# Optimization experiments

Hardware: AMD Instinct MI355X
Metric: run time of the kernel (lower is better)

## Reference

```python
import jax, jax.numpy as jnp
import numpy as np

TEMP = 0.07


def setup_inputs() -> dict:
    key = jax.random.key(0)
    k1, k2 = jax.random.split(key)
    N, C = 8192, 512
    X = jax.random.normal(k1, (N, C), dtype=jnp.float32)
    Y = jax.random.normal(k2, (N, C), dtype=jnp.float32)
    return {"X": X, "Y": Y}


def reference(X, Y):
    # Original loop computes, per row i, cross-entropy over logits
    # [X_i.Y_i, X_i.Y_j (j != i)] / temp with label 0 (the positive).
    # Softmax CE is permutation-invariant, so this equals
    #   logsumexp(S_i / temp) - S_ii / temp,  S = X @ Y^T,
    # summed over rows (loop accumulates with +=, i.e. sum reduction).
    S = jnp.einsum('nc,mc->nm', X, Y) / TEMP  # [N, N]
    lse = jax.nn.logsumexp(S, axis=1)          # [N]
    pos = jnp.diagonal(S)                      # [N]
    return jnp.sum(lse - pos)
```

## Files before the change

### kernel.cpp

```cpp
#include <hip/hip_runtime.h>
#include <stdint.h>

#define N 8192
#define C 512
#define BM 128
#define BN 128
#define NSPLIT 8
#define COLS_PER_SPLIT (N / NSPLIT)
#define CT (COLS_PER_SPLIT / BN)
#define GRID_GEMM (64 * NSPLIT)
#define KSTEPS (C / 64)
#define U_SCALE 20.609929155556617f
#define LN2 0.6931471805599453f

typedef __attribute__((ext_vector_type(4)))  int   i32x4;
typedef __attribute__((ext_vector_type(8)))  int   i32x8;
typedef __attribute__((ext_vector_type(16))) float f32x16;

__global__ __launch_bounds__(256) void prep_kernel(const float* __restrict__ X,
                                                   const float* __restrict__ Y,
                                                   unsigned char* __restrict__ Xf8,
                                                   unsigned char* __restrict__ Yf8,
                                                   float* __restrict__ pos) {
  const int wave = threadIdx.x >> 6;
  const int lane = threadIdx.x & 63;
  const int row = blockIdx.x * 4 + wave;
  const float4* xr = (const float4*)(X + (size_t)row * C) + lane * 2;
  const float4* yr = (const float4*)(Y + (size_t)row * C) + lane * 2;
  float4 x0 = xr[0], x1 = xr[1];
  float4 y0 = yr[0], y1 = yr[1];
  float s = x0.x * y0.x + x0.y * y0.y + x0.z * y0.z + x0.w * y0.w
          + x1.x * y1.x + x1.y * y1.y + x1.z * y1.z + x1.w * y1.w;
  int2 ox, oy;
  ox.x = __builtin_amdgcn_cvt_pk_fp8_f32(x0.x, x0.y, 0, false);
  ox.x = __builtin_amdgcn_cvt_pk_fp8_f32(x0.z, x0.w, ox.x, true);
  ox.y = __builtin_amdgcn_cvt_pk_fp8_f32(x1.x, x1.y, 0, false);
  ox.y = __builtin_amdgcn_cvt_pk_fp8_f32(x1.z, x1.w, ox.y, true);
  oy.x = __builtin_amdgcn_cvt_pk_fp8_f32(y0.x, y0.y, 0, false);
  oy.x = __builtin_amdgcn_cvt_pk_fp8_f32(y0.z, y0.w, oy.x, true);
  oy.y = __builtin_amdgcn_cvt_pk_fp8_f32(y1.x, y1.y, 0, false);
  oy.y = __builtin_amdgcn_cvt_pk_fp8_f32(y1.z, y1.w, oy.y, true);
  ((int2*)(Xf8 + (size_t)row * C))[lane] = ox;
  ((int2*)(Yf8 + (size_t)row * C))[lane] = oy;
#pragma unroll
  for (int off = 32; off >= 1; off >>= 1) s += __shfl_xor(s, off);
  if (lane == 0) pos[row] = s * U_SCALE;
}

__global__ __launch_bounds__(256, 2) void gemm_lse_kernel(const unsigned char* __restrict__ Xf8,
                                                          const unsigned char* __restrict__ Yf8,
                                                          float2* __restrict__ partials) {
  __shared__ unsigned char Bs[4096 * 16];

  const int tid = threadIdx.x;
  const int bx = blockIdx.x;
  const int split = bx & (NSPLIT - 1);
  const int rb = bx >> 3;
  const int row0 = rb * BM;
  const int colbase = split * COLS_PER_SPLIT;

  const int w = tid >> 6;
  const int lane = tid & 63;
  const int lrow = lane & 31;
  const int h = lane >> 5;
  const int arow = w * 32 + lrow;

  i32x8 a_frag[KSTEPS];
#pragma unroll
  for (int s = 0; s < KSTEPS; ++s) {
    const unsigned char* ga = Xf8 + (size_t)(row0 + arow) * C + s * 64 + h * 32;
    i32x4 lo = *(const i32x4*)ga;
    i32x4 hi = *(const i32x4*)(ga + 16);
    a_frag[s] = i32x8{ lo[0], lo[1], lo[2], lo[3], hi[0], hi[1], hi[2], hi[3] };
  }

  float m_s[16], l_s[16];
#pragma unroll
  for (int s = 0; s < 16; ++s) { m_s[s] = -INFINITY; l_s[s] = 0.0f; }

  const unsigned char* bsr = &Bs[0] + lane * 16;

  for (int ct = 0; ct < CT; ++ct) {
    const int col0 = colbase + ct * BN;
    f32x16 acc[4];
#pragma unroll
    for (int t = 0; t < 4; ++t)
#pragma unroll
      for (int e = 0; e < 16; ++e) acc[t][e] = 0.0f;

#pragma unroll
    for (int t = 0; t < 16; ++t) {
      const int L  = t * 256 + tid;
      const int l6 = L & 63;
      const int q  = (L >> 6) & 1;
      const int tj = (L >> 7) & 3;
      const int s  = L >> 9;
      const unsigned char* gb = Yf8
          + (size_t)(col0 + tj * 32 + (l6 & 31)) * C
          + s * 64 + (l6 >> 5) * 32 + q * 16;
      uint32_t loff = (uint32_t)((t * 256 + (tid & ~63)) * 16);
      __builtin_amdgcn_global_load_lds(
          (const __attribute__((address_space(1))) uint32_t*)(uintptr_t)gb,
          (__attribute__((address_space(3))) uint32_t*)(uintptr_t)((char*)&Bs[0] + loff),
          16, 0, 0);
    }
    __syncthreads();

#pragma unroll
    for (int s = 0; s < KSTEPS; ++s) {
#pragma unroll
      for (int tj = 0; tj < 4; ++tj) {
        i32x4 blo = *(const i32x4*)(bsr + (s * 4 + tj) * 2048);
        i32x4 bhi = *(const i32x4*)(bsr + (s * 4 + tj) * 2048 + 1024);
        i32x8 bf = { blo[0], blo[1], blo[2], blo[3], bhi[0], bhi[1], bhi[2], bhi[3] };
        acc[tj] = __builtin_amdgcn_mfma_scale_f32_32x32x64_f8f6f4(
            a_frag[s], bf, acc[tj], 0, 0, 0, 127, 0, 127);
      }
    }

#pragma unroll
    for (int r = 0; r < 16; ++r) {
      float v0 = acc[0][r] * U_SCALE;
      float v1 = acc[1][r] * U_SCALE;
      float v2 = acc[2][r] * U_SCALE;
      float v3 = acc[3][r] * U_SCALE;
      float mx = fmaxf(fmaxf(v0, v1), fmaxf(v2, v3));
      float mn = fmaxf(m_s[r], mx);
      l_s[r] = l_s[r] * exp2f(m_s[r] - mn)
             + exp2f(v0 - mn) + exp2f(v1 - mn) + exp2f(v2 - mn) + exp2f(v3 - mn);
      m_s[r] = mn;
    }
    __syncthreads();
  }

#pragma unroll
  for (int r = 0; r < 16; ++r) {
    float m = m_s[r], l = l_s[r];
#pragma unroll
    for (int off = 1; off < 32; off <<= 1) {
      float mo = __shfl_xor(m, off);
      float lo = __shfl_xor(l, off);
      float mn = fmaxf(m, mo);
      l = l * exp2f(m - mn) + lo * exp2f(mo - mn);
      m = mn;
    }
    m_s[r] = m; l_s[r] = l;
  }
  if (lrow == 0) {
#pragma unroll
    for (int r = 0; r < 16; ++r) {
      int row_local = (r & 3) + 8 * (r >> 2) + 4 * h;
      partials[(size_t)split * N + (row0 + w * 32 + row_local)] =
          make_float2(m_s[r], l_s[r]);
    }
  }
}

__global__ __launch_bounds__(256) void combine_kernel(const float2* __restrict__ partials,
                                                      const float* __restrict__ pos,
                                                      float* __restrict__ out) {
  int row = blockIdx.x * 256 + threadIdx.x;
  float M = -INFINITY, L = 0.0f;
#pragma unroll
  for (int s = 0; s < NSPLIT; ++s) {
    float2 pr = partials[(size_t)s * N + row];
    float mn = fmaxf(M, pr.x);
    L = L * exp2f(M - mn) + pr.y * exp2f(pr.x - mn);
    M = mn;
  }
  float v = M + __log2f(L) - pos[row];
#pragma unroll
  for (int off = 32; off >= 1; off >>= 1) v += __shfl_xor(v, off);
  __shared__ float wsum[4];
  if ((threadIdx.x & 63) == 0) wsum[threadIdx.x >> 6] = v;
  __syncthreads();
  if (threadIdx.x == 0)
    atomicAdd(out, LN2 * (wsum[0] + wsum[1] + wsum[2] + wsum[3]));
}

extern "C" void kernel_launch(void* const* d_in, const int* in_sizes, int n_in,
                              void* d_out, int out_size, void* d_ws, size_t ws_size,
                              hipStream_t stream) {
  const float* X = (const float*)d_in[0];
  const float* Y = (const float*)d_in[1];
  float* out = (float*)d_out;

  char* w = (char*)d_ws;
  unsigned char* Xf8 = (unsigned char*)w;
  unsigned char* Yf8 = Xf8 + (size_t)N * C;
  float2* partials = (float2*)(Yf8 + (size_t)N * C);
  float* pos = (float*)((char*)partials + (size_t)NSPLIT * N * sizeof(float2));

  hipMemsetAsync(d_out, 0, sizeof(float), stream);
  prep_kernel<<<N / 4, 256, 0, stream>>>(X, Y, Xf8, Yf8, pos);
  gemm_lse_kernel<<<GRID_GEMM, 256, 0, stream>>>(Xf8, Yf8, partials);
  combine_kernel<<<N / 256, 256, 0, stream>>>(partials, pos, out);
}
```

Baseline: 138.0 us.

## Double-buffer B tile in halves with swizzled row-major LDS layout

```diff
diff --git a/kernel.cpp b/kernel.cpp
--- a/kernel.cpp
+++ b/kernel.cpp
@@ -12,6 +12,7 @@
 #define KSTEPS (C / 64)
 #define U_SCALE 20.609929155556617f
 #define LN2 0.6931471805599453f
+#define WAITCNT_VM0 0x0F70
 
 typedef __attribute__((ext_vector_type(4)))  int   i32x4;
 typedef __attribute__((ext_vector_type(8)))  int   i32x8;
@@ -50,7 +51,7 @@
 __global__ __launch_bounds__(256, 2) void gemm_lse_kernel(const unsigned char* __restrict__ Xf8,
                                                           const unsigned char* __restrict__ Yf8,
                                                           float2* __restrict__ partials) {
-  __shared__ unsigned char Bs[4096 * 16];
+  __shared__ unsigned char Bs[2][BN * 256];
 
   const int tid = threadIdx.x;
   const int bx = blockIdx.x;
@@ -64,6 +65,7 @@
   const int lrow = lane & 31;
   const int h = lane >> 5;
   const int arow = w * 32 + lrow;
+  const int swz = lrow & 7;
 
   i32x8 a_frag[KSTEPS];
 #pragma unroll
@@ -78,43 +80,63 @@
 #pragma unroll
   for (int s = 0; s < 16; ++s) { m_s[s] = -INFINITY; l_s[s] = 0.0f; }
 
-  const unsigned char* bsr = &Bs[0] + lane * 16;
-
+  const int st_r  = tid >> 4;
+  const int st_c  = tid & 15;
+  const int st_sg = st_c >> 3;
+  const int st_j  = (st_c & 7) ^ (st_r & 7);
+
+  #define STAGE_PHASE(c, hf, b)                                                     \
+    {                                                                               \
+      const int col0_ = colbase + (c) * BN;                                         \
+      _Pragma("unroll")                                                             \
+      for (int i = 0; i < 8; ++i) {                                                 \
+        const int r_ = i * 16 + st_r;                                               \
+        const unsigned char* gb_ = Yf8 + (size_t)(col0_ + r_) * C                   \
+            + (hf) * 256 + st_sg * 128 + st_j * 16;                                 \
+        uint32_t loff_ = (uint32_t)((i * 256 + (tid & ~63)) * 16);                  \
+        __builtin_amdgcn_global_load_lds(                                           \
+            (const __attribute__((address_space(1))) uint32_t*)(uintptr_t)gb_,      \
+            (__attribute__((address_space(3))) uint32_t*)(uintptr_t)                \
+                ((char*)&Bs[b][0] + loff_),                                         \
+            16, 0, 0);                                                              \
+      }                                                                             \
+    }
+
+  STAGE_PHASE(0, 0, 0)
+
+  f32x16 acc[4];
+#pragma unroll 1
   for (int ct = 0; ct < CT; ++ct) {
-    const int col0 = colbase + ct * BN;
-    f32x16 acc[4];
 #pragma unroll
     for (int t = 0; t < 4; ++t)
 #pragma unroll
       for (int e = 0; e < 16; ++e) acc[t][e] = 0.0f;
 
 #pragma unroll
-    for (int t = 0; t < 16; ++t) {
-      const int L  = t * 256 + tid;
-      const int l6 = L & 63;
-      const int q  = (L >> 6) & 1;
-      const int tj = (L >> 7) & 3;
-      const int s  = L >> 9;
-      const unsigned char* gb = Yf8
-          + (size_t)(col0 + tj * 32 + (l6 & 31)) * C
-          + s * 64 + (l6 >> 5) * 32 + q * 16;
-      uint32_t loff = (uint32_t)((t * 256 + (tid & ~63)) * 16);
-      __builtin_amdgcn_global_load_lds(
-          (const __attribute__((address_space(1))) uint32_t*)(uintptr_t)gb,
-          (__attribute__((address_space(3))) uint32_t*)(uintptr_t)((char*)&Bs[0] + loff),
-          16, 0, 0);
-    }
-    __syncthreads();
-
-#pragma unroll
-    for (int s = 0; s < KSTEPS; ++s) {
-#pragma unroll
-      for (int tj = 0; tj < 4; ++tj) {
-        i32x4 blo = *(const i32x4*)(bsr + (s * 4 + tj) * 2048);
-        i32x4 bhi = *(const i32x4*)(bsr + (s * 4 + tj) * 2048 + 1024);
-        i32x8 bf = { blo[0], blo[1], blo[2], blo[3], bhi[0], bhi[1], bhi[2], bhi[3] };
-        acc[tj] = __builtin_amdgcn_mfma_scale_f32_32x32x64_f8f6f4(
-            a_frag[s], bf, acc[tj], 0, 0, 0, 127, 0, 127);
+    for (int half = 0; half < 2; ++half) {
+      const int p = ct * 2 + half;
+      __builtin_amdgcn_s_waitcnt(WAITCNT_VM0);
+      __builtin_amdgcn_s_barrier();
+      if (p + 1 < 2 * CT) {
+        const int nct = (p + 1) >> 1;
+        const int nhf = (p + 1) & 1;
+        STAGE_PHASE(nct, nhf, nhf)
+      }
+      const unsigned char* buf = &Bs[half][0];
+#pragma unroll
+      for (int sl = 0; sl < 4; ++sl) {
+        const int s = half * 4 + sl;
+        const int seg = (sl >> 1) * 128;
+        const int c0 = (sl & 1) * 4 + 2 * h;
+#pragma unroll
+        for (int tj = 0; tj < 4; ++tj) {
+          const int brow = tj * 32 + lrow;
+          i32x4 blo = *(const i32x4*)(buf + brow * 256 + seg + (((c0    ) ^ swz) * 16));
+          i32x4 bhi = *(const i32x4*)(buf + brow * 256 + seg + (((c0 + 1) ^ swz) * 16));
+          i32x8 bf = { blo[0], blo[1], blo[2], blo[3], bhi[0], bhi[1], bhi[2], bhi[3] };
+          acc[tj] = __builtin_amdgcn_mfma_scale_f32_32x32x64_f8f6f4(
+              a_frag[s], bf, acc[tj], 0, 0, 0, 127, 0, 127);
+        }
       }
     }
 
@@ -130,8 +152,8 @@
              + exp2f(v0 - mn) + exp2f(v1 - mn) + exp2f(v2 - mn) + exp2f(v3 - mn);
       m_s[r] = mn;
     }
-    __syncthreads();
-  }
+  }
+  #undef STAGE_PHASE
 
 #pragma unroll
   for (int r = 0; r < 16; ++r) {
```

Measured after the change: 134.5 us. -2.5%, faster.

## Load B fragments directly from global into registers, drop LDS staging

Applied to the files above, without the earlier changes.

```diff
diff --git a/kernel.cpp b/kernel.cpp
--- a/kernel.cpp
+++ b/kernel.cpp
@@ -50,12 +50,10 @@
 __global__ __launch_bounds__(256, 2) void gemm_lse_kernel(const unsigned char* __restrict__ Xf8,
                                                           const unsigned char* __restrict__ Yf8,
                                                           float2* __restrict__ partials) {
-  __shared__ unsigned char Bs[4096 * 16];
-
   const int tid = threadIdx.x;
   const int bx = blockIdx.x;
-  const int split = bx & (NSPLIT - 1);
-  const int rb = bx >> 3;
+  const int split = bx >> 6;
+  const int rb = bx & 63;
   const int row0 = rb * BM;
   const int colbase = split * COLS_PER_SPLIT;
 
@@ -78,10 +76,10 @@
 #pragma unroll
   for (int s = 0; s < 16; ++s) { m_s[s] = -INFINITY; l_s[s] = 0.0f; }
 
-  const unsigned char* bsr = &Bs[0] + lane * 16;
-
   for (int ct = 0; ct < CT; ++ct) {
     const int col0 = colbase + ct * BN;
+    const unsigned char* bbase = Yf8 + (size_t)(col0 + lrow) * C + h * 32;
+
     f32x16 acc[4];
 #pragma unroll
     for (int t = 0; t < 4; ++t)
@@ -89,33 +87,19 @@
       for (int e = 0; e < 16; ++e) acc[t][e] = 0.0f;
 
 #pragma unroll
-    for (int t = 0; t < 16; ++t) {
-      const int L  = t * 256 + tid;
-      const int l6 = L & 63;
-      const int q  = (L >> 6) & 1;
-      const int tj = (L >> 7) & 3;
-      const int s  = L >> 9;
-      const unsigned char* gb = Yf8
-          + (size_t)(col0 + tj * 32 + (l6 & 31)) * C
-          + s * 64 + (l6 >> 5) * 32 + q * 16;
-      uint32_t loff = (uint32_t)((t * 256 + (tid & ~63)) * 16);
-      __builtin_amdgcn_global_load_lds(
-          (const __attribute__((address_space(1))) uint32_t*)(uintptr_t)gb,
-          (__attribute__((address_space(3))) uint32_t*)(uintptr_t)((char*)&Bs[0] + loff),
-          16, 0, 0);
-    }
-    __syncthreads();
-
-#pragma unroll
     for (int s = 0; s < KSTEPS; ++s) {
+      i32x8 bf[4];
 #pragma unroll
       for (int tj = 0; tj < 4; ++tj) {
-        i32x4 blo = *(const i32x4*)(bsr + (s * 4 + tj) * 2048);
-        i32x4 bhi = *(const i32x4*)(bsr + (s * 4 + tj) * 2048 + 1024);
-        i32x8 bf = { blo[0], blo[1], blo[2], blo[3], bhi[0], bhi[1], bhi[2], bhi[3] };
+        const unsigned char* bp = bbase + (size_t)tj * 32 * C + s * 64;
+        i32x4 blo = *(const i32x4*)bp;
+        i32x4 bhi = *(const i32x4*)(bp + 16);
+        bf[tj] = i32x8{ blo[0], blo[1], blo[2], blo[3], bhi[0], bhi[1], bhi[2], bhi[3] };
+      }
+#pragma unroll
+      for (int tj = 0; tj < 4; ++tj)
         acc[tj] = __builtin_amdgcn_mfma_scale_f32_32x32x64_f8f6f4(
-            a_frag[s], bf, acc[tj], 0, 0, 0, 127, 0, 127);
-      }
+            a_frag[s], bf[tj], acc[tj], 0, 0, 0, 127, 0, 127);
     }
 
 #pragma unroll
@@ -130,7 +114,7 @@
              + exp2f(v0 - mn) + exp2f(v1 - mn) + exp2f(v2 - mn) + exp2f(v3 - mn);
       m_s[r] = mn;
     }
-    __syncthreads();
+    __builtin_amdgcn_s_barrier();
   }
 
 #pragma unroll
```

Result: slower. 222.4 us (+61.2%).
